# Performance work log

Hardware: AMD Instinct MI355X
Metric: run time of the kernel (lower is better)

Reference implementation:

```python
import jax, jax.numpy as jnp
import numpy as np

B, S, D = 2, 2048, 1024
NH, HD = 16, 64
MLP = 4096
EPS = 1e-6  # flax nnx.RMSNorm default epsilon


def rms_norm(x, scale):
    var = jnp.mean(jnp.square(x.astype(jnp.float32)), axis=-1, keepdims=True)
    return (x * jax.lax.rsqrt(var + EPS)).astype(x.dtype) * scale


def setup_inputs() -> dict:
    key = jax.random.key(0)
    ks = jax.random.split(key, 16)
    lin = lambda k, fin, fout: jax.random.normal(k, (fin, fout), jnp.float32) / np.sqrt(fin)
    x = jax.random.normal(ks[0], (B, S, D), jnp.float32)
    # causal mask [b, s, s]
    mask = jnp.broadcast_to(jnp.tril(jnp.ones((S, S), jnp.bool_))[None], (B, S, S))
    return {
        "x": x,
        "mask": mask,
        "attn_norm_scale": jnp.ones((D,), jnp.float32),
        "q_w": lin(ks[1], D, D), "q_b": jnp.zeros((D,), jnp.float32),
        "k_w": lin(ks[2], D, D), "k_b": jnp.zeros((D,), jnp.float32),
        "v_w": lin(ks[3], D, D), "v_b": jnp.zeros((D,), jnp.float32),
        "o_w": lin(ks[4], D, D), "o_b": jnp.zeros((D,), jnp.float32),
        "ffn_norm_scale": jnp.ones((D,), jnp.float32),
        "gate_w": lin(ks[5], D, MLP), "gate_b": jnp.zeros((MLP,), jnp.float32),
        "up_w": lin(ks[6], D, MLP), "up_b": jnp.zeros((MLP,), jnp.float32),
        "down_w": lin(ks[7], MLP, D), "down_b": jnp.zeros((D,), jnp.float32),
    }


def reference(x, mask, attn_norm_scale, q_w, q_b, k_w, k_b, v_w, v_b, o_w, o_b,
              ffn_norm_scale, gate_w, gate_b, up_w, up_b, down_w, down_b):
    b, s, d = x.shape
    h = rms_norm(x, attn_norm_scale)
    q = (h @ q_w + q_b).reshape(b, s, NH, HD)
    k = (h @ k_w + k_b).reshape(b, s, NH, HD)
    v = (h @ v_w + v_b).reshape(b, s, NH, HD)
    scale = jnp.float32(HD) ** -0.5
    logits = jnp.einsum('bsnh,btnh->bnst', q, k) * scale  # [b, n, s, s]
    logits = jnp.where(mask[:, None, :, :], logits, jnp.finfo(logits.dtype).min)
    attn = jax.nn.softmax(logits.astype(jnp.float32), axis=-1).astype(x.dtype)
    attn_out = jnp.einsum('bnst,btnh->bsnh', attn, v).reshape(b, s, d)
    x = x + attn_out @ o_w + o_b
    h = rms_norm(x, ffn_norm_scale)
    ffn = (jax.nn.silu(h @ gate_w + gate_b) * (h @ up_w + up_b)) @ down_w + down_b
    return x + ffn
```

## Files before the change

### kernel.cpp

```cpp
#include <hip/hip_runtime.h>

#define S_LEN 2048
#define DMODEL 1024
#define NHEADS 16
#define MLPDIM 4096

typedef float f32x4 __attribute__((ext_vector_type(4)));
typedef __bf16 bf16x8 __attribute__((ext_vector_type(8)));
typedef __bf16 bf16x4 __attribute__((ext_vector_type(4)));

__device__ __forceinline__ void gload_lds16(const void* gsrc, void* ldst) {
  __builtin_amdgcn_global_load_lds(
      (const __attribute__((address_space(1))) void*)gsrc,
      (__attribute__((address_space(3))) void*)ldst, 16, 0, 0);
}

#define BARR() __builtin_amdgcn_s_barrier()
#define VMC(n) do { asm volatile("s_waitcnt vmcnt(" #n ")" ::: "memory"); __builtin_amdgcn_sched_barrier(0); } while (0)

__global__ __launch_bounds__(256) void prep_k(
    const float* __restrict__ qw, const float* __restrict__ kw,
    const float* __restrict__ vw, const float* __restrict__ ow,
    const float* __restrict__ gw, const float* __restrict__ uw,
    const float* __restrict__ dw, __bf16* __restrict__ wqkv,
    __bf16* __restrict__ wo, __bf16* __restrict__ wg, __bf16* __restrict__ wu,
    __bf16* __restrict__ wd, const float* __restrict__ qb,
    const float* __restrict__ kb, const float* __restrict__ vb,
    float* __restrict__ bqkv, const float* __restrict__ x,
    const float* __restrict__ ascale, __bf16* __restrict__ hbuf) {
  __shared__ __bf16 tile[64][66];
  __shared__ float part[4];
  int bid = blockIdx.x, t = threadIdx.x;
  if (bid >= 8192) {
    int i = (bid - 8192) * 256 + t;
    if (i < 1024) bqkv[i] = qb[i];
    else if (i < 2048) bqkv[i] = kb[i - 1024];
    else if (i < 3072) bqkv[i] = vb[i - 2048];
    return;
  }
  if (bid >= 4096) {
    int row = bid - 4096;
    f32x4 v = ((const f32x4*)(x + (size_t)row * DMODEL))[t];
    float ss = v[0] * v[0] + v[1] * v[1] + v[2] * v[2] + v[3] * v[3];
#pragma unroll
    for (int off = 1; off < 64; off <<= 1) ss += __shfl_xor(ss, off, 64);
    if ((t & 63) == 0) part[t >> 6] = ss;
    __syncthreads();
    float tot = part[0] + part[1] + part[2] + part[3];
    float r = rsqrtf(tot * (1.0f / DMODEL) + 1e-6f);
    f32x4 s4 = ((const f32x4*)ascale)[t];
    bf16x4 o;
#pragma unroll
    for (int e = 0; e < 4; ++e) o[e] = (__bf16)(v[e] * r * s4[e]);
    ((bf16x4*)hbuf)[(size_t)row * (DMODEL / 4) + t] = o;
    return;
  }
  const float* in;
  __bf16* out;
  int K, N, bx, by;
  if (bid < 1024) {
    int job = bid >> 8, tt = bid & 255;
    K = 1024; N = 1024; bx = tt & 15; by = tt >> 4;
    in = (job == 0) ? qw : (job == 1) ? kw : (job == 2) ? vw : ow;
    out = (job == 0) ? wqkv : (job == 1) ? wqkv + 1024 * 1024
        : (job == 2) ? wqkv + 2 * 1024 * 1024 : wo;
  } else if (bid < 3072) {
    int job = (bid - 1024) >> 10, tt = (bid - 1024) & 1023;
    K = 1024; N = 4096; bx = tt & 63; by = tt >> 6;
    in = job ? uw : gw;
    out = job ? wu : wg;
  } else {
    int tt = bid - 3072;
    K = 4096; N = 1024; bx = tt & 15; by = tt >> 4;
    in = dw; out = wd;
  }
  int n0 = bx * 64, k0 = by * 64;
  int rr = (t & 63) >> 4, sl = t & 15, wv = t >> 6;
#pragma unroll
  for (int j = 0; j < 4; ++j) {
    int r = wv * 4 + rr + j * 16;
    f32x4 v = *(const f32x4*)(in + (size_t)(k0 + r) * N + n0 + sl * 4);
#pragma unroll
    for (int e = 0; e < 4; ++e) tile[r][sl * 4 + e] = (__bf16)v[e];
  }
  __syncthreads();
#pragma unroll
  for (int j = 0; j < 2; ++j) {
    int u = t + j * 256;
    int n = u >> 3, kc = u & 7;
    bf16x8 o;
#pragma unroll
    for (int e = 0; e < 8; ++e) o[e] = tile[kc * 8 + e][n];
    *(bf16x8*)(out + (size_t)(n0 + n) * K + k0 + kc * 8) = o;
  }
}

__global__ __launch_bounds__(256) void vtrans_k(
    const __bf16* __restrict__ qkv, __bf16* __restrict__ vt) {
  __shared__ __bf16 tile[32][33];
  int s0 = blockIdx.x * 32, c0 = blockIdx.y * 32, b = blockIdx.z;
  int tx = threadIdx.x & 31, ty = threadIdx.x >> 5;
#pragma unroll
  for (int r = 0; r < 32; r += 8)
    tile[r + ty][tx] = qkv[(size_t)(b * S_LEN + s0 + r + ty) * 3072 + 2048 + c0 + tx];
  __syncthreads();
  int hf = (tx >> 4) & 1, g4q = (tx >> 2) & 3, r2 = tx & 3;
  int txp = g4q * 8 + hf * 4 + r2;
#pragma unroll
  for (int r = 0; r < 32; r += 8)
    vt[(size_t)(b * 1024 + c0 + r + ty) * S_LEN + s0 + txp] = tile[tx][r + ty];
}

__global__ __launch_bounds__(256) void rmsnorm_k(
    const float* __restrict__ x, const float* __restrict__ scale,
    __bf16* __restrict__ out) {
  int row = blockIdx.x, tid = threadIdx.x;
  f32x4 v = ((const f32x4*)(x + (size_t)row * DMODEL))[tid];
  float ss = v[0] * v[0] + v[1] * v[1] + v[2] * v[2] + v[3] * v[3];
#pragma unroll
  for (int off = 1; off < 64; off <<= 1) ss += __shfl_xor(ss, off, 64);
  __shared__ float part[4];
  if ((tid & 63) == 0) part[tid >> 6] = ss;
  __syncthreads();
  float tot = part[0] + part[1] + part[2] + part[3];
  float r = rsqrtf(tot * (1.0f / DMODEL) + 1e-6f);
  f32x4 s4 = ((const f32x4*)scale)[tid];
  bf16x4 o;
#pragma unroll
  for (int e = 0; e < 4; ++e) o[e] = (__bf16)(v[e] * r * s4[e]);
  ((bf16x4*)out)[(size_t)row * (DMODEL / 4) + tid] = o;
}

__global__ __launch_bounds__(256, 4) void gemm_gu(
    const __bf16* __restrict__ A, const __bf16* __restrict__ Gt,
    const __bf16* __restrict__ Ut, const float* __restrict__ gb,
    const float* __restrict__ ub, __bf16* __restrict__ Cout,
    int M, int N, int K) {
  __shared__ __attribute__((aligned(16))) __bf16 As[128 * 64];
  __shared__ __attribute__((aligned(16))) __bf16 Gs[64 * 64];
  __shared__ __attribute__((aligned(16))) __bf16 Us[64 * 64];
  int tid = threadIdx.x, lane = tid & 63, wave = tid >> 6;
  int l15 = lane & 15, g4 = lane >> 4;
  int lin = blockIdx.x;
  int xcd = lin & 7, idx = lin >> 3;
  int bxl = idx >> 4, byl = idx & 15;
  int bn = ((xcd & 3) * 16 + bxl) * 64;
  int bm = ((xcd >> 2) * 16 + byl) * 128;
  int wr = wave >> 1, wc = wave & 1;
  f32x4 ag[4][2] = {}, au[4][2] = {};
  const __bf16* Abase = A + (size_t)bm * K;
  const __bf16* Gbase = Gt + (size_t)bn * K;
  const __bf16* Ubase = Ut + (size_t)bn * K;

  for (int k0 = 0; k0 < K; k0 += 64) {
#pragma unroll
    for (int j = 0; j < 4; ++j) {
      int u = tid + j * 256;
      int r = u >> 3, c = (u & 7) ^ (r & 7);
      gload_lds16(Abase + (size_t)r * K + k0 + c * 8, As + u * 8);
    }
#pragma unroll
    for (int j = 0; j < 2; ++j) {
      int u = tid + j * 256;
      int r = u >> 3, c = (u & 7) ^ (r & 7);
      gload_lds16(Gbase + (size_t)r * K + k0 + c * 8, Gs + u * 8);
      gload_lds16(Ubase + (size_t)r * K + k0 + c * 8, Us + u * 8);
    }
    __syncthreads();
#pragma unroll
    for (int ks = 0; ks < 2; ++ks) {
      bf16x8 af[4], gf[2], uf[2];
#pragma unroll
      for (int m = 0; m < 4; ++m) {
        int r = wr * 64 + m * 16 + l15;
        af[m] = *(const bf16x8*)(As + r * 64 + (((4 * ks + g4) ^ (r & 7)) << 3));
      }
#pragma unroll
      for (int n = 0; n < 2; ++n) {
        int r = wc * 32 + n * 16 + l15;
        int off = r * 64 + (((4 * ks + g4) ^ (r & 7)) << 3);
        gf[n] = *(const bf16x8*)(Gs + off);
        uf[n] = *(const bf16x8*)(Us + off);
      }
      __builtin_amdgcn_s_setprio(1);
#pragma unroll
      for (int m = 0; m < 4; ++m)
#pragma unroll
        for (int n = 0; n < 2; ++n) {
          ag[m][n] = __builtin_amdgcn_mfma_f32_16x16x32_bf16(af[m], gf[n], ag[m][n], 0, 0, 0);
          au[m][n] = __builtin_amdgcn_mfma_f32_16x16x32_bf16(af[m], uf[n], au[m][n], 0, 0, 0);
        }
      __builtin_amdgcn_s_setprio(0);
    }
    __syncthreads();
  }
  int r0 = bm + wr * 64 + g4 * 4;
  int c0 = bn + wc * 32 + l15;
#pragma unroll
  for (int n = 0; n < 2; ++n) {
    int c = c0 + n * 16;
    float gbv = gb[c], ubv = ub[c];
#pragma unroll
    for (int m = 0; m < 4; ++m) {
      int rb = r0 + m * 16;
#pragma unroll
      for (int rg = 0; rg < 4; ++rg) {
        float g = ag[m][n][rg] + gbv;
        float u = au[m][n][rg] + ubv;
        float v = g / (1.0f + __expf(-g)) * u;
        Cout[(size_t)(rb + rg) * N + c] = (__bf16)v;
      }
    }
  }
}

template <int OUT_BF16, int RESID, int SILU>
__global__ __launch_bounds__(256, 3) void gemm_n64(
    const __bf16* __restrict__ A, const __bf16* __restrict__ Bt,
    const float* __restrict__ bias, const float* __restrict__ resid,
    const __bf16* __restrict__ aux, void* __restrict__ Cout,
    int M, int N, int K) {
  __shared__ __attribute__((aligned(16))) __bf16 As[2][128 * 64];
  __shared__ __attribute__((aligned(16))) __bf16 Bs[2][64 * 64];
  int tid = threadIdx.x, lane = tid & 63, wave = tid >> 6;
  int l15 = lane & 15, g4 = lane >> 4;
  int NB = N >> 6;
  int xcd = blockIdx.x & 7, j = blockIdx.x >> 3;
  int grp = j / (2 * NB), jj = j - grp * 2 * NB;
  int bm = (xcd * (M >> 10) + grp * 2 + (jj & 1)) * 128;
  int bn = (jj >> 1) * 64;
  int wr = wave >> 1, wc = wave & 1;
  f32x4 acc[4][2] = {};
  const __bf16* Abase = A + (size_t)bm * K;
  const __bf16* Bbase = Bt + (size_t)bn * K;

  auto stage = [&](int k0, int sb) {
#pragma unroll
    for (int i = 0; i < 4; ++i) {
      int u = tid + i * 256;
      int r = u >> 3, c = (u & 7) ^ (r & 7);
      gload_lds16(Abase + (size_t)r * K + k0 + c * 8, As[sb] + u * 8);
    }
#pragma unroll
    for (int i = 0; i < 2; ++i) {
      int u = tid + i * 256;
      int r = u >> 3, c = (u & 7) ^ (r & 7);
      gload_lds16(Bbase + (size_t)r * K + k0 + c * 8, Bs[sb] + u * 8);
    }
  };

  int NT = K >> 6;
  stage(0, 0);
  for (int t = 0; t < NT; ++t) {
    int sb = t & 1;
    if (t + 1 < NT) { stage((t + 1) << 6, sb ^ 1); VMC(6); }
    else { VMC(0); }
    BARR();
#pragma unroll
    for (int ks = 0; ks < 2; ++ks) {
      bf16x8 af[4], bfr[2];
#pragma unroll
      for (int m = 0; m < 4; ++m) {
        int r = wr * 64 + m * 16 + l15;
        af[m] = *(const bf16x8*)(As[sb] + r * 64 + (((4 * ks + g4) ^ (r & 7)) << 3));
      }
#pragma unroll
      for (int n = 0; n < 2; ++n) {
        int r = wc * 32 + n * 16 + l15;
        bfr[n] = *(const bf16x8*)(Bs[sb] + r * 64 + (((4 * ks + g4) ^ (r & 7)) << 3));
      }
      __builtin_amdgcn_s_setprio(1);
#pragma unroll
      for (int m = 0; m < 4; ++m)
#pragma unroll
        for (int n = 0; n < 2; ++n)
          acc[m][n] = __builtin_amdgcn_mfma_f32_16x16x32_bf16(af[m], bfr[n], acc[m][n], 0, 0, 0);
      __builtin_amdgcn_s_setprio(0);
    }
    BARR();
  }
  int r0 = bm + wr * 64 + g4 * 4;
  int c0 = bn + wc * 32 + l15;
#pragma unroll
  for (int n = 0; n < 2; ++n) {
    int c = c0 + n * 16;
    float bv = bias[c];
#pragma unroll
    for (int m = 0; m < 4; ++m) {
      int rb = r0 + m * 16;
#pragma unroll
      for (int rg = 0; rg < 4; ++rg) {
        int r = rb + rg;
        size_t idx = (size_t)r * N + c;
        float v = acc[m][n][rg] + bv;
        if (SILU) {
          float gg = (float)aux[idx];
          v *= gg / (1.0f + __expf(-gg));
        }
        if (RESID) v += resid[idx];
        if (OUT_BF16) ((__bf16*)Cout)[idx] = (__bf16)v;
        else ((float*)Cout)[idx] = v;
      }
    }
  }
}

#define SCL2E 0.180336879f
__global__ __launch_bounds__(512, 4) void attn_k(
    const __bf16* __restrict__ qkv, const __bf16* __restrict__ vt,
    __bf16* __restrict__ ao) {
  __shared__ __attribute__((aligned(16))) __bf16 Ks[2][128 * 64];
  __shared__ __attribute__((aligned(16))) __bf16 Vs[2][64 * 128];
  int tid = threadIdx.x, lane = tid & 63, w = tid >> 6;
  int l15 = lane & 15, g4 = lane >> 4;
  int bh = blockIdx.x, b = bh >> 4, h = bh & 15;
  int qt = 15 - blockIdx.y;
  int qb = qt * 128;
  int qw = qb + w * 16;
  const __bf16* qkvb = qkv + (size_t)b * S_LEN * 3072 + h * 64;
  const __bf16* kgb = qkvb + 1024;
  const __bf16* vtb = vt + (size_t)b * 1024 * S_LEN + (size_t)(h * 64) * S_LEN;

  bf16x8 qf[2];
#pragma unroll
  for (int ks = 0; ks < 2; ++ks)
    qf[ks] = *(const bf16x8*)(qkvb + (size_t)(qw + l15) * 3072 + 32 * ks + 8 * g4);

  f32x4 oa[4] = {};
  float mrow = -1e30f, lrow = 0.f;
  int q = qw + l15;
  int nt = qt + 1;

  auto stage = [&](int kvb, int buf) {
#pragma unroll
    for (int i = 0; i < 2; ++i) {
      int u = tid + i * 512;
      int r = u >> 3, c = u & 7;
      gload_lds16(kgb + (size_t)(kvb + r) * 3072 + ((c ^ (r & 7)) << 3),
                  Ks[buf] + w * 512 + i * 4096);
    }
#pragma unroll
    for (int i = 0; i < 2; ++i) {
      int u = tid + i * 512;
      int r = u >> 4, cu = u & 15;
      gload_lds16(vtb + (size_t)r * S_LEN + kvb + ((cu ^ (r & 7)) << 3),
                  Vs[buf] + w * 512 + i * 4096);
    }
  };

  stage(0, 0);
  __syncthreads();
  int buf = 0;
  for (int t = 0; t < nt; ++t) {
    int kvb = t * 128;
    if (t + 1 < nt) stage(kvb + 128, buf ^ 1);

    f32x4 sa[8];
#pragma unroll
    for (int i = 0; i < 8; ++i) sa[i] = f32x4{0.f, 0.f, 0.f, 0.f};
#pragma unroll
    for (int st = 0; st < 2; ++st)
#pragma unroll
      for (int ks = 0; ks < 2; ++ks) {
        bf16x8 kf[4];
#pragma unroll
        for (int n = 0; n < 4; ++n) {
          int rr = st * 64 + n * 16 + l15;
          int bc = (64 * ks + 16 * g4) ^ ((rr & 7) << 4);
          kf[n] = *(const bf16x8*)((const char*)Ks[buf] + rr * 128 + bc);
        }
        __builtin_amdgcn_s_setprio(1);
#pragma unroll
        for (int n = 0; n < 4; ++n)
          sa[st * 4 + n] = __builtin_amdgcn_mfma_f32_16x16x32_bf16(kf[n], qf[ks], sa[st * 4 + n], 0, 0, 0);
        __builtin_amdgcn_s_setprio(0);
      }

    bool lastt = (t == nt - 1);
    float nmx = -1e30f;
#pragma unroll
    for (int i = 0; i < 8; ++i)
#pragma unroll
      for (int rg = 0; rg < 4; ++rg) {
        float s = sa[i][rg] * SCL2E;
        if (lastt) {
          int key = kvb + (i >> 2) * 64 + (i & 3) * 16 + 4 * g4 + rg;
          s = (key <= q) ? s : -1e30f;
        }
        sa[i][rg] = s;
        nmx = fmaxf(nmx, s);
      }
    nmx = fmaxf(nmx, __shfl_xor(nmx, 16));
    nmx = fmaxf(nmx, __shfl_xor(nmx, 32));
    float nm;
    if (!__all(nmx <= mrow)) {
      nm = fmaxf(mrow, nmx);
      float sc = exp2f(mrow - nm);
      mrow = nm;
      lrow *= sc;
#pragma unroll
      for (int rg = 0; rg < 4; ++rg) {
        float scq = __shfl(sc, 4 * g4 + rg);
#pragma unroll
        for (int dn = 0; dn < 4; ++dn) oa[dn][rg] *= scq;
      }
    } else {
      nm = mrow;
    }
    float rs = 0.f;
    bf16x8 pa[2][2];
#pragma unroll
    for (int st = 0; st < 2; ++st)
#pragma unroll
      for (int ks = 0; ks < 2; ++ks)
#pragma unroll
        for (int hf = 0; hf < 2; ++hf)
#pragma unroll
          for (int rg = 0; rg < 4; ++rg) {
            float p = exp2f(sa[st * 4 + 2 * ks + hf][rg] - nm);
            rs += p;
            pa[st][ks][hf * 4 + rg] = (__bf16)p;
          }
    rs += __shfl_xor(rs, 16);
    rs += __shfl_xor(rs, 32);
    lrow += rs;

#pragma unroll
    for (int st = 0; st < 2; ++st)
#pragma unroll
      for (int ks = 0; ks < 2; ++ks) {
        __builtin_amdgcn_s_setprio(1);
#pragma unroll
        for (int dn = 0; dn < 4; ++dn) {
          int rr = dn * 16 + l15;
          int swz = (rr & 7) << 4;
          const char* vrow = (const char*)Vs[buf] + rr * 256;
          bf16x8 vf = *(const bf16x8*)(vrow + ((st * 128 + ks * 64 + g4 * 16) ^ swz));
          oa[dn] = __builtin_amdgcn_mfma_f32_16x16x32_bf16(pa[st][ks], vf, oa[dn], 0, 0, 0);
        }
        __builtin_amdgcn_s_setprio(0);
      }
    __syncthreads();
    buf ^= 1;
  }

  __bf16* aobase = ao + (size_t)b * S_LEN * DMODEL + h * 64;
#pragma unroll
  for (int rg = 0; rg < 4; ++rg) {
    float rl = 1.0f / __shfl(lrow, 4 * g4 + rg);
    int qo = qw + 4 * g4 + rg;
#pragma unroll
    for (int dn = 0; dn < 4; ++dn)
      aobase[(size_t)qo * DMODEL + dn * 16 + l15] = (__bf16)(oa[dn][rg] * rl);
  }
}

#define OFF_WQKV 0
#define OFF_WO 6291456
#define OFF_WG 8388608
#define OFF_WU 16777216
#define OFF_WD 25165824
#define OFF_BQKV 33554432
#define OFF_H 33570816
#define OFF_QKV 41959424
#define OFF_AO 67125248
#define OFF_T 75513856
#define OFF_VT OFF_T
#define OFF_X2 109068288

extern "C" void kernel_launch(void* const* d_in, const int* in_sizes, int n_in,
                              void* d_out, int out_size, void* d_ws, size_t ws_size,
                              hipStream_t stream) {
  (void)in_sizes; (void)n_in; (void)out_size; (void)ws_size;
  const float* x = (const float*)d_in[0];
  const float* attn_scale = (const float*)d_in[2];
  const float* q_w = (const float*)d_in[3];
  const float* q_b = (const float*)d_in[4];
  const float* k_w = (const float*)d_in[5];
  const float* k_b = (const float*)d_in[6];
  const float* v_w = (const float*)d_in[7];
  const float* v_b = (const float*)d_in[8];
  const float* o_w = (const float*)d_in[9];
  const float* o_b = (const float*)d_in[10];
  const float* ffn_scale = (const float*)d_in[11];
  const float* gate_w = (const float*)d_in[12];
  const float* gate_b = (const float*)d_in[13];
  const float* up_w = (const float*)d_in[14];
  const float* up_b = (const float*)d_in[15];
  const float* down_w = (const float*)d_in[16];
  const float* down_b = (const float*)d_in[17];

  char* ws = (char*)d_ws;
  __bf16* wqkv = (__bf16*)(ws + OFF_WQKV);
  __bf16* wo = (__bf16*)(ws + OFF_WO);
  __bf16* wg = (__bf16*)(ws + OFF_WG);
  __bf16* wu = (__bf16*)(ws + OFF_WU);
  __bf16* wd = (__bf16*)(ws + OFF_WD);
  float* bqkv = (float*)(ws + OFF_BQKV);
  __bf16* hbuf = (__bf16*)(ws + OFF_H);
  __bf16* qkvbuf = (__bf16*)(ws + OFF_QKV);
  __bf16* aobuf = (__bf16*)(ws + OFF_AO);
  __bf16* tbuf = (__bf16*)(ws + OFF_T);
  __bf16* vtbuf = (__bf16*)(ws + OFF_VT);
  float* x2 = (float*)(ws + OFF_X2);

  dim3 blk(256);
  prep_k<<<dim3(8204), blk, 0, stream>>>(q_w, k_w, v_w, o_w, gate_w, up_w, down_w,
                                         wqkv, wo, wg, wu, wd, q_b, k_b, v_b, bqkv,
                                         x, attn_scale, hbuf);
  gemm_n64<1, 0, 0><<<dim3(1536), blk, 0, stream>>>(hbuf, wqkv, bqkv, nullptr, nullptr, qkvbuf, 4096, 3072, 1024);
  vtrans_k<<<dim3(64, 32, 2), blk, 0, stream>>>(qkvbuf, vtbuf);
  attn_k<<<dim3(32, 16), dim3(512), 0, stream>>>(qkvbuf, vtbuf, aobuf);
  gemm_n64<0, 1, 0><<<dim3(512), blk, 0, stream>>>(aobuf, wo, o_b, x, nullptr, x2, 4096, 1024, 1024);
  rmsnorm_k<<<4096, blk, 0, stream>>>(x2, ffn_scale, hbuf);
  gemm_gu<<<dim3(2048), blk, 0, stream>>>(hbuf, wg, wu, gate_b, up_b, tbuf, 4096, 4096, 1024);
  gemm_n64<0, 1, 0><<<dim3(512), blk, 0, stream>>>(tbuf, wd, down_b, x2, nullptr, (float*)d_out, 4096, 1024, 4096);
}
```

Baseline: 250.5 us.

## Fuse V transpose into a dedicated 128x128 QKV GEMM epilogue

Replaces the generic 128x64-tile QKV GEMM plus the separate V-transpose kernel with a new 128x128-tile GEMM that writes Q/K normally and writes V directly in the transposed, permuted layout the attention kernel expects. This removes one kernel launch and a full read/write pass over V, and the larger tile raises data reuse. The cost is a single-buffered K loop with no prefetch, lower occupancy (launch bounds 3), and scattered 8-byte stores for the V tiles.

```diff
diff --git a/kernel.cpp b/kernel.cpp
--- a/kernel.cpp
+++ b/kernel.cpp
@@ -95,22 +95,6 @@
   }
 }
 
-__global__ __launch_bounds__(256) void vtrans_k(
-    const __bf16* __restrict__ qkv, __bf16* __restrict__ vt) {
-  __shared__ __bf16 tile[32][33];
-  int s0 = blockIdx.x * 32, c0 = blockIdx.y * 32, b = blockIdx.z;
-  int tx = threadIdx.x & 31, ty = threadIdx.x >> 5;
-#pragma unroll
-  for (int r = 0; r < 32; r += 8)
-    tile[r + ty][tx] = qkv[(size_t)(b * S_LEN + s0 + r + ty) * 3072 + 2048 + c0 + tx];
-  __syncthreads();
-  int hf = (tx >> 4) & 1, g4q = (tx >> 2) & 3, r2 = tx & 3;
-  int txp = g4q * 8 + hf * 4 + r2;
-#pragma unroll
-  for (int r = 0; r < 32; r += 8)
-    vt[(size_t)(b * 1024 + c0 + r + ty) * S_LEN + s0 + txp] = tile[tx][r + ty];
-}
-
 __global__ __launch_bounds__(256) void rmsnorm_k(
     const float* __restrict__ x, const float* __restrict__ scale,
     __bf16* __restrict__ out) {
@@ -129,6 +113,82 @@
 #pragma unroll
   for (int e = 0; e < 4; ++e) o[e] = (__bf16)(v[e] * r * s4[e]);
   ((bf16x4*)out)[(size_t)row * (DMODEL / 4) + tid] = o;
+}
+
+__global__ __launch_bounds__(256, 3) void gemm_qkv(
+    const __bf16* __restrict__ A, const __bf16* __restrict__ Bt,
+    const float* __restrict__ bias, __bf16* __restrict__ C,
+    __bf16* __restrict__ vt, int M, int N, int K) {
+  __shared__ __attribute__((aligned(16))) __bf16 As[128 * 64];
+  __shared__ __attribute__((aligned(16))) __bf16 Bs[128 * 64];
+  int tid = threadIdx.x, lane = tid & 63, wave = tid >> 6;
+  int l15 = lane & 15, g4 = lane >> 4;
+  int NB = N >> 7, P = M >> 10;
+  int xcd = blockIdx.x & 7, j = blockIdx.x >> 3;
+  int grp = j / (2 * NB), jj = j - grp * 2 * NB;
+  int bm = (xcd * P + grp * 2 + (jj & 1)) * 128;
+  int bn = (jj >> 1) * 128;
+  int wr = wave >> 1, wc = wave & 1;
+  f32x4 acc[4][4] = {};
+  const __bf16* Abase = A + (size_t)bm * K;
+  const __bf16* Bbase = Bt + (size_t)bn * K;
+
+  for (int k0 = 0; k0 < K; k0 += 64) {
+#pragma unroll
+    for (int i = 0; i < 4; ++i) {
+      int u = tid + i * 256;
+      int r = u >> 3, c = (u & 7) ^ (r & 7);
+      gload_lds16(Abase + (size_t)r * K + k0 + c * 8, As + u * 8);
+      gload_lds16(Bbase + (size_t)r * K + k0 + c * 8, Bs + u * 8);
+    }
+    __syncthreads();
+#pragma unroll
+    for (int ks = 0; ks < 2; ++ks) {
+      bf16x8 af[4], bfr[4];
+#pragma unroll
+      for (int m = 0; m < 4; ++m) {
+        int r = wr * 64 + m * 16 + l15;
+        af[m] = *(const bf16x8*)(As + r * 64 + (((4 * ks + g4) ^ (r & 7)) << 3));
+      }
+#pragma unroll
+      for (int n = 0; n < 4; ++n) {
+        int r = wc * 64 + n * 16 + l15;
+        bfr[n] = *(const bf16x8*)(Bs + r * 64 + (((4 * ks + g4) ^ (r & 7)) << 3));
+      }
+      __builtin_amdgcn_s_setprio(1);
+#pragma unroll
+      for (int m = 0; m < 4; ++m)
+#pragma unroll
+        for (int n = 0; n < 4; ++n)
+          acc[m][n] = __builtin_amdgcn_mfma_f32_16x16x32_bf16(af[m], bfr[n], acc[m][n], 0, 0, 0);
+      __builtin_amdgcn_s_setprio(0);
+    }
+    __syncthreads();
+  }
+  int r0 = bm + wr * 64 + g4 * 4;
+  int c0 = bn + wc * 64 + l15;
+  bool isV = (bn >= 2048);
+#pragma unroll
+  for (int n = 0; n < 4; ++n) {
+    int c = c0 + n * 16;
+    float bv = bias[c];
+#pragma unroll
+    for (int m = 0; m < 4; ++m) {
+      int rb = r0 + m * 16;
+      if (!isV) {
+#pragma unroll
+        for (int rg = 0; rg < 4; ++rg)
+          C[(size_t)(rb + rg) * N + c] = (__bf16)(acc[m][n][rg] + bv);
+      } else {
+        bf16x4 vv;
+#pragma unroll
+        for (int rg = 0; rg < 4; ++rg) vv[rg] = (__bf16)(acc[m][n][rg] + bv);
+        int b = rb >> 11, s = rb & 2047;
+        int sp = (s & ~31) | (((s >> 2) & 3) << 3) | (((s >> 4) & 1) << 2);
+        *(bf16x4*)(vt + (size_t)(b * 1024 + c - 2048) * S_LEN + sp) = vv;
+      }
+    }
+  }
 }
 
 __global__ __launch_bounds__(256, 4) void gemm_gu(
@@ -508,8 +568,7 @@
   prep_k<<<dim3(8204), blk, 0, stream>>>(q_w, k_w, v_w, o_w, gate_w, up_w, down_w,
                                          wqkv, wo, wg, wu, wd, q_b, k_b, v_b, bqkv,
                                          x, attn_scale, hbuf);
-  gemm_n64<1, 0, 0><<<dim3(1536), blk, 0, stream>>>(hbuf, wqkv, bqkv, nullptr, nullptr, qkvbuf, 4096, 3072, 1024);
-  vtrans_k<<<dim3(64, 32, 2), blk, 0, stream>>>(qkvbuf, vtbuf);
+  gemm_qkv<<<dim3(768), blk, 0, stream>>>(hbuf, wqkv, bqkv, qkvbuf, vtbuf, 4096, 3072, 1024);
   attn_k<<<dim3(32, 16), dim3(512), 0, stream>>>(qkvbuf, vtbuf, aobuf);
   gemm_n64<0, 1, 0><<<dim3(512), blk, 0, stream>>>(aobuf, wo, o_b, x, nullptr, x2, 4096, 1024, 1024);
   rmsnorm_k<<<4096, blk, 0, stream>>>(x2, ffn_scale, hbuf);
```

After: 240.8 us (median of 5 runs). -3.9%, faster.
